# Optimization experiments

Measured on AMD Instinct MI355X. Metric: run time of the kernel, lower is better.

The kernel has to match this reference:

```python
import jax, jax.numpy as jnp
import numpy as np

# Straight-through-estimator round (round_pass in the original code)
def _round_ste(x):
    return x + jax.lax.stop_gradient(jnp.round(x) - x)

INPUT_QMAX = 127.0   # 2**(input_bit-1)-1,  input_bit=8
WEIGHT_QMAX = 127.0  # 2**(weight_bit-1)-1, weight_bit=8
OUT_RANGE = 127.0    # 2**(output_bit-1)-1, output_bit=8


def setup_inputs() -> dict:
    key = jax.random.key(0)
    k0, k1, k2 = jax.random.split(key, 3)
    B, Cin, Cout, H, W, K = 16, 320, 320, 64, 64, 3
    x = jax.random.normal(k0, (B, Cin, H, W), dtype=jnp.float32)
    weight = jax.random.normal(k1, (Cout, Cin, K, K), dtype=jnp.float32) * 0.05
    bias = jax.random.normal(k2, (Cout,), dtype=jnp.float32) * 0.1
    # LSQ learned scalar step sizes (cloned from conv_lsq in the original)
    step_x = jnp.float32(0.02)
    step_w = jnp.float32(0.002)
    step_b = jnp.float32(0.01)
    # Bit_shift_layer scale: shift conv accumulator down into output_bit range
    shift_scale = jnp.float32(2.0 ** -7)
    return {"x": x, "weight": weight, "bias": bias, "step_x": step_x,
            "step_w": step_w, "step_b": step_b, "shift_scale": shift_scale}


def reference(x, weight, bias, step_x, step_w, step_b, shift_scale):
    # --- lsq_quant_input (isint=True): x_int in [-127,127], x_scale = 1/step ---
    x_int = jnp.clip(_round_ste(x / step_x), -INPUT_QMAX, INPUT_QMAX)
    x_scale = 1.0 / step_x
    # --- lsq_quant_weight (isint=True) ---
    w_int = jnp.clip(_round_ste(weight / step_w), -WEIGHT_QMAX, WEIGHT_QMAX)
    w_scale = 1.0 / step_w
    # --- Conv2d_int: integer-valued conv (no bias) ---
    y_int = jax.lax.conv_general_dilated(
        x_int, w_int, window_strides=(1, 1), padding=((1, 1), (1, 1)),
        dimension_numbers=("NCHW", "OIHW", "NCHW"))
    # --- mvm_result_shift: bit-shift accumulator into output range ---
    y_shift = jnp.clip(_round_ste(y_int * shift_scale), -OUT_RANGE, OUT_RANGE)
    # --- lsq_quant_bias (isint=False): dequantized bias ---
    b_deq = jnp.clip(_round_ste(bias / step_b), -OUT_RANGE, OUT_RANGE) * step_b
    # --- bias requant to output int scale, add, clamp (fused epilogue) ---
    b_int8 = jnp.clip(_round_ste(b_deq * shift_scale * x_scale * w_scale),
                      -OUT_RANGE, OUT_RANGE)
    y_shift_dmac = jnp.clip(y_shift + b_int8[None, :, None, None],
                            -OUT_RANGE, OUT_RANGE)
    # module returns y_shift_DMAC (the integer-valued clamped output)
    return y_shift_dmac
```

## Files before the change

kernel.cpp:

```cpp
#include <hip/hip_runtime.h>

typedef int v4i  __attribute__((ext_vector_type(4)));
typedef int v16i __attribute__((ext_vector_type(16)));

#define QMAX 127.0f

#define XQ_BYTES 22302720
#define WQ_BYTES 921600

__device__ __forceinline__ float clampf(float v, float lo, float hi) {
    return fminf(fmaxf(v, lo), hi);
}

__device__ __forceinline__ float qround(float v, float step, float inv) {
    float t = v * inv;
    float r = rintf(t);
    float d = fabsf(t - r);
    if (fabsf(d - 0.5f) < fabsf(t) * 1e-5f + 1e-5f)
        r = rintf(v / step);
    return r;
}

__device__ __forceinline__ void gload_lds16(const char* g, char* l) {
    __builtin_amdgcn_global_load_lds(
        (const __attribute__((address_space(1))) void*)g,
        (__attribute__((address_space(3))) void*)l, 16, 0, 0);
}

__device__ __forceinline__ v16i mfma32_i8(v4i a, v4i b, v16i c) {
    return __builtin_amdgcn_mfma_i32_32x32x32_i8(a, b, c, 0, 0, 0);
}

__global__ __launch_bounds__(256) void fused_prep_kernel(
    const float* __restrict__ x, const float* __restrict__ w,
    const float* __restrict__ bias,
    const float* __restrict__ step_x_p, const float* __restrict__ step_w_p,
    const float* __restrict__ step_b_p, const float* __restrict__ shift_p,
    char* __restrict__ xq, char* __restrict__ wq2, float* __restrict__ bi)
{
    __shared__ float F[32 * 289];
    const int bid = blockIdx.x;
    const int t = threadIdx.x;

    if (bid < 1024) {
        const int h = bid & 63;
        const int b = bid >> 6;
        const float step = *step_x_p;
        const float inv  = 1.0f / step;
        const int wcol = t >> 2;
        const int cg   = t & 3;
        v4i vals[5];

        for (int c5 = 0; c5 < 5; ++c5) {
            {
                const int r = t >> 4, c = (t & 15) * 4;
                const float* src = x + (((size_t)(b * 320 + c5 * 64) * 64 + h) * 64);
#pragma unroll
                for (int i = 0; i < 4; ++i) {
                    const int row = r + i * 16;
                    *(float4*)&F[row * 65 + c] =
                        *(const float4*)(src + (size_t)row * 4096 + c);
                }
            }
            __syncthreads();
            int dws[4];
#pragma unroll
            for (int j = 0; j < 4; ++j) {
                int word = 0;
#pragma unroll
                for (int k = 0; k < 4; ++k) {
                    float v = F[(cg * 16 + j * 4 + k) * 65 + wcol];
                    int xi = (int)clampf(qround(v, step, inv), -QMAX, QMAX);
                    word |= (xi & 0xFF) << (8 * k);
                }
                dws[j] = word;
            }
            vals[c5] = (v4i){dws[0], dws[1], dws[2], dws[3]};
            __syncthreads();
        }

        const int col = wcol + 1;
        const int key = ((col >> 1) & 1) << 1;
        char* base = xq + ((size_t)(b * 66 + (h + 1)) * 66 + col) * 320;
#pragma unroll
        for (int c5 = 0; c5 < 5; ++c5)
            *(v4i*)(base + c5 * 64 + (((cg ^ key)) << 4)) = vals[c5];

    } else if (bid < 1124) {
        const int blk = bid - 1024;
        const int cot = blk / 10;
        const int rem = blk - cot * 10;
        const int c5  = rem >> 1;
        const int ks  = rem & 1;
        const float step = *step_w_p;
        const float inv  = 1.0f / step;

        for (int idx = t; idx < 2304; idx += 256) {
            const int co_l = idx / 72;
            const int m4   = idx - co_l * 72;
            const float4 v = *(const float4*)(
                w + (size_t)(cot * 32 + co_l) * 2880 + c5 * 576 + ks * 288 + m4 * 4);
            float* dst = &F[co_l * 289 + m4 * 4];
            dst[0] = v.x; dst[1] = v.y; dst[2] = v.z; dst[3] = v.w;
        }
        __syncthreads();

        const int co_l = (t >> 2) & 31;
        const int cib  = (t >> 7) * 16 + (t & 3) * 4;
        char* dst = wq2 + (size_t)(c5 * 20 + ks * 10 + cot) * 1024 + t * 4;
#pragma unroll
        for (int p = 0; p < 9; ++p) {
            int word = 0;
#pragma unroll
            for (int k = 0; k < 4; ++k) {
                float v = F[co_l * 289 + (cib + k) * 9 + p];
                int q = (int)clampf(qround(v, step, inv), -QMAX, QMAX);
                word |= (q & 0xFF) << (8 * k);
            }
            *(int*)(dst + (size_t)p * 102400) = word;
        }
    } else if (bid < 1449) {
        int tid = (bid - 1124) * 256 + t;
        if (tid < 83200) {
            int b = tid / 5200;
            int r = tid - b * 5200;
            int px = r / 20;
            int ck = (r - px * 20) * 16;
            int row, col;
            if (px < 66)       { row = 0;  col = px; }
            else if (px < 132) { row = 65; col = px - 66; }
            else { int e = px - 132; row = 1 + (e >> 1); col = (e & 1) * 65; }
            size_t off = ((size_t)(b * 66 + row) * 66 + col) * 320 + ck;
            v4i z = {0, 0, 0, 0};
            *(v4i*)&xq[off] = z;
        }
    } else {
        const float step_b = *step_b_p;
        const float xs = 1.0f / *step_x_p;
        const float ws = 1.0f / *step_w_p;
        const float shift = *shift_p;
#pragma unroll
        for (int co = t; co < 320; co += 256) {
            float b_deq = clampf(rintf(bias[co] / step_b), -QMAX, QMAX) * step_b;
            float v = ((b_deq * shift) * xs) * ws;
            bi[co] = clampf(rintf(v), -QMAX, QMAX);
        }
    }
}

__global__ __launch_bounds__(256, 3) void conv_mfma_kernel(
    const char* __restrict__ xq, const char* __restrict__ wq2,
    const float* __restrict__ bi, const float* __restrict__ shift_p,
    float* __restrict__ out)
{
    __shared__ __attribute__((aligned(16))) char B_lds[2][25344];

    const int t  = threadIdx.x;
    const int id = blockIdx.x;
    const int g  = id / 40;
    const int r  = id - g * 40;
    const int bx = r >> 3;
    const int ptile = (g << 3) | (r & 7);

    const int co0 = bx * 64;
    const int b  = ptile >> 4;
    const int h0 = (ptile & 15) * 4;

    const int wave = t >> 6, lane = t & 63;
    const int l31 = lane & 31, hi = lane >> 5;

    const char* xbase = xq + ((size_t)(b * 66 + h0) * 66) * 320;

    v16i acc[2][2] = {};

    for (int c = t; c < 1584; c += 256) {
        const char* gp = xbase + (c >> 2) * 320 + ((c & 3) << 4);
        gload_lds16(gp, &B_lds[0][(c - lane) * 16]);
    }
    __syncthreads();

    for (int c5 = 0; c5 < 5; ++c5) {
        if (c5 < 4) {
            const int ci0 = (c5 + 1) * 64;
            char* dst = B_lds[(c5 + 1) & 1];
            for (int c = t; c < 1584; c += 256) {
                const char* gp = xbase + (c >> 2) * 320 + ci0 + ((c & 3) << 4);
                gload_lds16(gp, &dst[(c - lane) * 16]);
            }
        }

        const char* Bc = B_lds[c5 & 1];
        const char* wp = wq2 + (c5 * 20 + bx * 2) * 1024 + lane * 16;

        v4i areg[2][2][2];
#pragma unroll
        for (int ct = 0; ct < 2; ++ct)
#pragma unroll
            for (int ks = 0; ks < 2; ++ks)
                areg[0][ct][ks] = *(const v4i*)(wp + ks * 10240 + ct * 1024);

#pragma unroll
        for (int p = 0; p < 9; ++p) {
            const int dh = p / 3, dw = p - dh * 3;
            if (p < 8) {
#pragma unroll
                for (int ct = 0; ct < 2; ++ct)
#pragma unroll
                    for (int ks = 0; ks < 2; ++ks)
                        areg[(p + 1) & 1][ct][ks] = *(const v4i*)(
                            wp + (p + 1) * 102400 + ks * 10240 + ct * 1024);
            }
            const int prow = wave + dh;
            v4i bf[2][2];
#pragma unroll
            for (int h = 0; h < 2; ++h) {
                const int col = h * 32 + l31 + dw;
                const int p2  = (col >> 1) & 1;
                const int base = (prow * 66 + col) * 64 + (hi << 4);
#pragma unroll
                for (int ks = 0; ks < 2; ++ks)
                    bf[h][ks] = *(const v4i*)&Bc[base + ((ks ^ p2) << 5)];
            }
            __builtin_amdgcn_s_setprio(1);
#pragma unroll
            for (int ks = 0; ks < 2; ++ks)
#pragma unroll
                for (int h = 0; h < 2; ++h)
#pragma unroll
                    for (int ct = 0; ct < 2; ++ct)
                        acc[ct][h] = mfma32_i8(areg[p & 1][ct][ks], bf[h][ks],
                                               acc[ct][h]);
            __builtin_amdgcn_s_setprio(0);
        }
        __syncthreads();
    }

    const float shift = *shift_p;
    const int h = h0 + wave;
#pragma unroll
    for (int ct = 0; ct < 2; ++ct) {
#pragma unroll
        for (int reg = 0; reg < 16; ++reg) {
            const int row = (reg & 3) + 8 * (reg >> 2) + 4 * hi;
            const int co = co0 + ct * 32 + row;
            const float bv = bi[co];
            float* orow = out + (((size_t)(b * 320 + co) * 64) + h) * 64;
#pragma unroll
            for (int hh = 0; hh < 2; ++hh) {
                float y  = (float)acc[ct][hh][reg];
                float ys = clampf(rintf(y * shift), -QMAX, QMAX);
                orow[hh * 32 + l31] = clampf(ys + bv, -QMAX, QMAX);
            }
        }
    }
}

extern "C" void kernel_launch(void* const* d_in, const int* in_sizes, int n_in,
                              void* d_out, int out_size, void* d_ws, size_t ws_size,
                              hipStream_t stream) {
    const float* x      = (const float*)d_in[0];
    const float* w      = (const float*)d_in[1];
    const float* bias   = (const float*)d_in[2];
    const float* step_x = (const float*)d_in[3];
    const float* step_w = (const float*)d_in[4];
    const float* step_b = (const float*)d_in[5];
    const float* shift  = (const float*)d_in[6];
    float* out = (float*)d_out;

    char*  xq  = (char*)d_ws;
    char*  wq2 = xq + XQ_BYTES;
    float* bi  = (float*)(wq2 + WQ_BYTES);

    fused_prep_kernel<<<1450, 256, 0, stream>>>(x, w, bias, step_x, step_w,
                                                step_b, shift, xq, wq2, bi);
    conv_mfma_kernel<<<1280, 256, 0, stream>>>(xq, wq2, bi, shift, out);
}
```

Before: 224.5 us.

## Re-layout quantized input as channel-chunk planes to remove LDS swizzle

```diff
diff --git a/kernel.cpp b/kernel.cpp
--- a/kernel.cpp
+++ b/kernel.cpp
@@ -80,11 +80,11 @@
         }
 
         const int col = wcol + 1;
-        const int key = ((col >> 1) & 1) << 1;
-        char* base = xq + ((size_t)(b * 66 + (h + 1)) * 66 + col) * 320;
+        char* base = xq + ((size_t)(b * 66 + (h + 1))) * 21120
+                   + (cg >> 1) * 2112 + col * 32 + (cg & 1) * 16;
 #pragma unroll
         for (int c5 = 0; c5 < 5; ++c5)
-            *(v4i*)(base + c5 * 64 + (((cg ^ key)) << 4)) = vals[c5];
+            *(v4i*)(base + c5 * 4224) = vals[c5];
 
     } else if (bid < 1124) {
         const int blk = bid - 1024;
@@ -125,12 +125,14 @@
             int b = tid / 5200;
             int r = tid - b * 5200;
             int px = r / 20;
-            int ck = (r - px * 20) * 16;
+            int pc = r - px * 20;
+            int c5 = pc >> 2, q = pc & 3;
             int row, col;
             if (px < 66)       { row = 0;  col = px; }
             else if (px < 132) { row = 65; col = px - 66; }
             else { int e = px - 132; row = 1 + (e >> 1); col = (e & 1) * 65; }
-            size_t off = ((size_t)(b * 66 + row) * 66 + col) * 320 + ck;
+            size_t off = ((size_t)(b * 66 + row)) * 21120 + c5 * 4224
+                       + (q >> 1) * 2112 + col * 32 + (q & 1) * 16;
             v4i z = {0, 0, 0, 0};
             *(v4i*)&xq[off] = z;
         }
@@ -169,22 +171,25 @@
     const int wave = t >> 6, lane = t & 63;
     const int l31 = lane & 31, hi = lane >> 5;
 
-    const char* xbase = xq + ((size_t)(b * 66 + h0) * 66) * 320;
+    const char* xbase = xq + (size_t)(b * 66 + h0) * 21120;
 
     v16i acc[2][2] = {};
 
     for (int c = t; c < 1584; c += 256) {
-        const char* gp = xbase + (c >> 2) * 320 + ((c & 3) << 4);
+        const int row = c / 264;
+        const int rem = c - row * 264;
+        const char* gp = xbase + row * 21120 + rem * 16;
         gload_lds16(gp, &B_lds[0][(c - lane) * 16]);
     }
     __syncthreads();
 
     for (int c5 = 0; c5 < 5; ++c5) {
         if (c5 < 4) {
-            const int ci0 = (c5 + 1) * 64;
             char* dst = B_lds[(c5 + 1) & 1];
             for (int c = t; c < 1584; c += 256) {
-                const char* gp = xbase + (c >> 2) * 320 + ci0 + ((c & 3) << 4);
+                const int row = c / 264;
+                const int rem = c - row * 264;
+                const char* gp = xbase + row * 21120 + (c5 + 1) * 4224 + rem * 16;
                 gload_lds16(gp, &dst[(c - lane) * 16]);
             }
         }
@@ -213,23 +218,22 @@
             const int prow = wave + dh;
             v4i bf[2][2];
 #pragma unroll
-            for (int h = 0; h < 2; ++h) {
-                const int col = h * 32 + l31 + dw;
-                const int p2  = (col >> 1) & 1;
-                const int base = (prow * 66 + col) * 64 + (hi << 4);
+            for (int h2 = 0; h2 < 2; ++h2) {
+                const int col = h2 * 32 + l31 + dw;
+                const int cbase = prow * 4224 + col * 32 + (hi << 4);
 #pragma unroll
                 for (int ks = 0; ks < 2; ++ks)
-                    bf[h][ks] = *(const v4i*)&Bc[base + ((ks ^ p2) << 5)];
+                    bf[h2][ks] = *(const v4i*)&Bc[cbase + ks * 2112];
             }
             __builtin_amdgcn_s_setprio(1);
 #pragma unroll
             for (int ks = 0; ks < 2; ++ks)
 #pragma unroll
-                for (int h = 0; h < 2; ++h)
+                for (int h2 = 0; h2 < 2; ++h2)
 #pragma unroll
                     for (int ct = 0; ct < 2; ++ct)
-                        acc[ct][h] = mfma32_i8(areg[p & 1][ct][ks], bf[h][ks],
-                                               acc[ct][h]);
+                        acc[ct][h2] = mfma32_i8(areg[p & 1][ct][ks], bf[h2][ks],
+                                                acc[ct][h2]);
             __builtin_amdgcn_s_setprio(0);
         }
         __syncthreads();
```

Measured after the change: 222.5 us. About the same (-0.9%).
